# Performance work log

Hardware: AMD Instinct MI355X
Metric: run time of the kernel (lower is better)

## Reference

```python
import jax, jax.numpy as jnp
import numpy as np

N, E_DIM, H, N_EDGES, OUT = 4096, 256, 4, 131072, 256


def _ln(x, g, b, eps=1e-5):
    m = x.mean(-1, keepdims=True)
    v = ((x - m) ** 2).mean(-1, keepdims=True)
    return (x - m) / jnp.sqrt(v + eps) * g + b


def _mha(q_in, kv_in, in_w, in_b, out_w, out_b, n_heads):
    # torch nn.MultiheadAttention with packed in_proj_weight [3E, E]
    e = q_in.shape[-1]
    dh = e // n_heads
    wq, wk, wv = jnp.split(in_w, 3, axis=0)
    bq, bk, bv = jnp.split(in_b, 3)
    q = (q_in @ wq.T + bq).reshape(-1, n_heads, dh)   # [N,H,Dh]
    k = (kv_in @ wk.T + bk).reshape(-1, n_heads, dh)
    v = (kv_in @ wv.T + bv).reshape(-1, n_heads, dh)
    scale = 1.0 / jnp.sqrt(jnp.asarray(dh, q.dtype))
    scores = jnp.einsum('nhd,mhd->hnm', q, k) * scale  # [H,N,M]
    attn = jax.nn.softmax(scores, axis=-1)
    o = jnp.einsum('hnm,mhd->nhd', attn, v).reshape(-1, e)
    return o @ out_w.T + out_b


def _gcn_conv(x, edge_index):
    # out[c] += (1/sqrt(d[c])) * (1/sqrt(d[r])) * x[r] for each edge (r,c),
    # d = in-degree counted on col; non-finite norms zeroed (nan_to_num)
    n = x.shape[0]
    row, col = edge_index[0], edge_index[1]
    d = jax.ops.segment_sum(jnp.ones_like(col, dtype=x.dtype), col, num_segments=n)
    dn = 1.0 / jnp.sqrt(d)
    value = dn[col] * dn[row]
    value = jnp.where(jnp.isfinite(value), value, 0.0)
    return jax.ops.segment_sum(value[:, None] * x[row], col, num_segments=n)


def setup_inputs() -> dict:
    key = jax.random.key(0)
    ks = jax.random.split(key, 12)
    s = 1.0 / np.sqrt(E_DIM)
    rn = lambda k, shape: jax.random.normal(k, shape, jnp.float32) * s
    return {
        'x': jax.random.normal(ks[0], (N, E_DIM), jnp.float32),
        'edge_index': jax.random.randint(ks[1], (2, N_EDGES), 0, N, dtype=jnp.int32),
        'weight_local': jax.random.uniform(ks[2], (E_DIM, E_DIM), jnp.float32, -s, s),
        'sa_in_w': rn(ks[3], (3 * E_DIM, E_DIM)),
        'sa_in_b': jnp.zeros((3 * E_DIM,), jnp.float32),
        'sa_out_w': rn(ks[4], (E_DIM, E_DIM)),
        'sa_out_b': jnp.zeros((E_DIM,), jnp.float32),
        'ln1_g': jnp.ones((E_DIM,), jnp.float32),
        'ln1_b': jnp.zeros((E_DIM,), jnp.float32),
        'ca_in_w': rn(ks[5], (3 * E_DIM, E_DIM)),
        'ca_in_b': jnp.zeros((3 * E_DIM,), jnp.float32),
        'ca_out_w': rn(ks[6], (E_DIM, E_DIM)),
        'ca_out_b': jnp.zeros((E_DIM,), jnp.float32),
        'ln2_g': jnp.ones((E_DIM,), jnp.float32),
        'ln2_b': jnp.zeros((E_DIM,), jnp.float32),
        'gate_w': rn(ks[7], (E_DIM, 2 * E_DIM)),
        'gate_b': jnp.zeros((E_DIM,), jnp.float32),
        'fc_w': rn(ks[8], (OUT, E_DIM)),
        'fc_b': jnp.zeros((OUT,), jnp.float32),
    }


def reference(x, edge_index, weight_local, sa_in_w, sa_in_b, sa_out_w, sa_out_b,
              ln1_g, ln1_b, ca_in_w, ca_in_b, ca_out_w, ca_out_b, ln2_g, ln2_b,
              gate_w, gate_b, fc_w, fc_b):
    hi = _gcn_conv(x, edge_index)                       # [N,E]
    local_embed = hi @ weight_local                     # [N,E]
    attn_out = _mha(x, x, sa_in_w, sa_in_b, sa_out_w, sa_out_b, H)
    global_embed = _ln(x + attn_out, ln1_g, ln1_b)      # [N,E]
    cross_out = _mha(global_embed, local_embed, ca_in_w, ca_in_b, ca_out_w, ca_out_b, H)
    aligned = _ln(global_embed + cross_out, ln2_g, ln2_b)
    concat = jnp.concatenate([global_embed, aligned], axis=-1)  # [N,2E]
    final_embed = jax.nn.relu(concat @ gate_w.T + gate_b)
    return final_embed @ fc_w.T + fc_b
```

## Files before the change

kernel.cpp:

```cpp
#include <hip/hip_runtime.h>
#include <hip/hip_bf16.h>

#define NN 4096
#define EDIM 256
#define NHEAD 4
#define DH 64
#define NEDGE 131072
#define NE (NN * EDIM)
#define NSPLIT 8
#define KEYS_PER_SPLIT (NN / NSPLIT)
#define QKS 512
#define QSCL 0.18033688011112042f

typedef __bf16 bf16x8 __attribute__((ext_vector_type(8)));
typedef float f32x4 __attribute__((ext_vector_type(4)));
typedef float f32x16 __attribute__((ext_vector_type(16)));

__device__ inline void gload_lds16(const void* g, void* l) {
    __builtin_amdgcn_global_load_lds((const __attribute__((address_space(1))) unsigned int*)g,
                                     (__attribute__((address_space(3))) unsigned int*)l, 16, 0, 0);
}

__global__ __launch_bounds__(256) void prep_kernel(
    const float* __restrict__ wl, const float* __restrict__ siw, const float* __restrict__ sib,
    const float* __restrict__ sow, const float* __restrict__ ciw, const float* __restrict__ cib,
    const float* __restrict__ cow, const float* __restrict__ gw, const float* __restrict__ fw,
    const float* __restrict__ x,
    __bf16* __restrict__ siwb, __bf16* __restrict__ ciwb, __bf16* __restrict__ sowb,
    __bf16* __restrict__ cowb, __bf16* __restrict__ gwb, __bf16* __restrict__ fwb,
    __bf16* __restrict__ wlT, __bf16* __restrict__ xb,
    float* __restrict__ sib_adj, float* __restrict__ cib_adj, int* __restrict__ degi) {
    long i = (long)blockIdx.x * 256 + threadIdx.x;
    if (i < 196608) { float v = siw[i]; if (i < 65536) v *= QSCL; siwb[i] = (__bf16)v; return; }
    i -= 196608;
    if (i < 196608) { float v = ciw[i]; if (i < 65536) v *= QSCL; ciwb[i] = (__bf16)v; return; }
    i -= 196608;
    if (i < 65536) { sowb[i] = (__bf16)sow[i]; return; }
    i -= 65536;
    if (i < 65536) { cowb[i] = (__bf16)cow[i]; return; }
    i -= 65536;
    if (i < 131072) { gwb[i] = (__bf16)gw[i]; return; }
    i -= 131072;
    if (i < 65536) { fwb[i] = (__bf16)fw[i]; return; }
    i -= 65536;
    if (i < 65536) { int n = (int)(i >> 8), k = (int)(i & 255); wlT[i] = (__bf16)wl[k * 256 + n]; return; }
    i -= 65536;
    if (i < 1048576) { xb[i] = (__bf16)x[i]; return; }
    i -= 1048576;
    if (i < 768) { sib_adj[i] = sib[i] * (i < 256 ? QSCL : 1.f); return; }
    i -= 768;
    if (i < 768) { cib_adj[i] = cib[i] * (i < 256 ? QSCL : 1.f); return; }
    i -= 768;
    if (i < 4096) degi[i] = 0;
}

__global__ __launch_bounds__(256) void degi_kernel(const int* __restrict__ ei,
                                                   int* __restrict__ degi, int ne) {
    int e = blockIdx.x * 256 + threadIdx.x;
    if (e < ne) atomicAdd(&degi[ei[ne + e]], 1);
}

__global__ __launch_bounds__(256) void scan_kernel(const int* __restrict__ degi,
                                                   int* __restrict__ off,
                                                   int* __restrict__ cursor,
                                                   float* __restrict__ dnz) {
    __shared__ int s[256];
    const int t = threadIdx.x, i0 = t * 16;
    int v[16], sum = 0;
#pragma unroll
    for (int j = 0; j < 16; ++j) { v[j] = degi[i0 + j]; sum += v[j]; }
    s[t] = sum;
    __syncthreads();
#pragma unroll
    for (int d = 1; d < 256; d <<= 1) {
        int add = (t >= d) ? s[t - d] : 0;
        __syncthreads();
        s[t] += add;
        __syncthreads();
    }
    int base = s[t] - sum;
#pragma unroll
    for (int j = 0; j < 16; ++j) {
        off[i0 + j] = base;
        cursor[i0 + j] = base;
        dnz[i0 + j] = (v[j] > 0) ? rsqrtf((float)v[j]) : 0.f;
        base += v[j];
    }
}

__global__ __launch_bounds__(256) void fill_kernel(const int* __restrict__ ei,
                                                   int* __restrict__ cursor,
                                                   int* __restrict__ rows, int ne) {
    int e = blockIdx.x * 256 + threadIdx.x;
    if (e < ne) {
        int r = ei[e], c = ei[ne + e];
        int pos = atomicAdd(&cursor[c], 1);
        rows[pos] = r;
    }
}

__global__ __launch_bounds__(256) void gather_kernel(const int* __restrict__ off,
                                                     const int* __restrict__ rows,
                                                     const float* __restrict__ dnz,
                                                     const __bf16* __restrict__ xb,
                                                     __bf16* __restrict__ hib) {
    __shared__ float sm[2][256];
    const int c = blockIdx.x, t = threadIdx.x;
    const int half = t >> 7, c2 = (t & 127) * 2;
    const int s0 = off[c];
    const int s1 = (c == NN - 1) ? NEDGE : off[c + 1];
    float a0 = 0.f, a1 = 0.f;
    for (int j = s0 + half; j < s1; j += 2) {
        int r = rows[j];
        float dv = dnz[r];
        unsigned int pk = *(const unsigned int*)&xb[(size_t)r * EDIM + c2];
        a0 += dv * __uint_as_float(pk << 16);
        a1 += dv * __uint_as_float(pk & 0xffff0000u);
    }
    sm[half][c2] = a0;
    sm[half][c2 + 1] = a1;
    __syncthreads();
    float v = (sm[0][t] + sm[1][t]) * dnz[c];
    hib[(size_t)c * EDIM + t] = (__bf16)v;
}

__device__ inline void gemm_core(const __bf16* __restrict__ A, int lda,
                                 const __bf16* __restrict__ Bt, int ldb,
                                 int row0, int col0, int K, int tid,
                                 __bf16* As, __bf16* Bs, f32x4 acc[4]) {
    const int w = tid >> 6, l = tid & 63, lr = l & 15, lk = l >> 4;
    const int srow = (l >> 3), scol = (l & 7) * 8;
    auto stage = [&](int k0, int buf) {
#pragma unroll
        for (int cc = 0; cc < 2; ++cc) {
            int E0 = (w * 2 + cc) * 512;
            int row = (E0 >> 6) + srow;
            int sc = scol ^ ((row & 7) << 3);
            gload_lds16(A + (size_t)(row0 + row) * lda + k0 + sc, &As[buf * 4096 + E0]);
            gload_lds16(Bt + (size_t)(col0 + row) * ldb + k0 + sc, &Bs[buf * 4096 + E0]);
        }
    };
    stage(0, 0);
    __syncthreads();
    int buf = 0;
    for (int k0 = 0; k0 < K; k0 += 64) {
        if (k0 + 64 < K) stage(k0 + 64, buf ^ 1);
#pragma unroll
        for (int ks = 0; ks < 2; ++ks) {
            int cswz = (ks * 32 + lk * 8) ^ ((lr & 7) << 3);
            bf16x8 af = *(bf16x8*)&As[buf * 4096 + (w * 16 + lr) * 64 + cswz];
#pragma unroll
            for (int nt = 0; nt < 4; ++nt) {
                bf16x8 bfr = *(bf16x8*)&Bs[buf * 4096 + (nt * 16 + lr) * 64 + cswz];
                acc[nt] = __builtin_amdgcn_mfma_f32_16x16x32_bf16(af, bfr, acc[nt], 0, 0, 0);
            }
        }
        __syncthreads();
        buf ^= 1;
    }
}

template <bool RELU, bool OUTBF>
__global__ __launch_bounds__(256) void gemm_bf16(const __bf16* __restrict__ A,
                                                 const __bf16* __restrict__ A2, int lda,
                                                 const __bf16* __restrict__ Bt, int ldb,
                                                 const float* __restrict__ bias,
                                                 void* __restrict__ Cv, int ldc, int K) {
    __shared__ __align__(16) __bf16 As[2 * 4096];
    __shared__ __align__(16) __bf16 Bs[2 * 4096];
    const int tid = threadIdx.x;
    const int row0 = blockIdx.y * 64, col0 = blockIdx.x * 64;
    const int w = tid >> 6, l = tid & 63, lr = l & 15, lk = l >> 4;
    const int srow = (l >> 3), scol = (l & 7) * 8;
    f32x4 acc[4] = {};
    auto stage = [&](int k0, int buf) {
        const __bf16* Asrc = A;
        int ka = k0;
        if (A2 != nullptr && k0 >= 256) { Asrc = A2; ka = k0 - 256; }
#pragma unroll
        for (int cc = 0; cc < 2; ++cc) {
            int E0 = (w * 2 + cc) * 512;
            int row = (E0 >> 6) + srow;
            int sc = scol ^ ((row & 7) << 3);
            gload_lds16(Asrc + (size_t)(row0 + row) * lda + ka + sc, &As[buf * 4096 + E0]);
            gload_lds16(Bt + (size_t)(col0 + row) * ldb + k0 + sc, &Bs[buf * 4096 + E0]);
        }
    };
    stage(0, 0);
    __syncthreads();
    int buf = 0;
    for (int k0 = 0; k0 < K; k0 += 64) {
        if (k0 + 64 < K) stage(k0 + 64, buf ^ 1);
#pragma unroll
        for (int ks = 0; ks < 2; ++ks) {
            int cswz = (ks * 32 + lk * 8) ^ ((lr & 7) << 3);
            bf16x8 af = *(bf16x8*)&As[buf * 4096 + (w * 16 + lr) * 64 + cswz];
#pragma unroll
            for (int nt = 0; nt < 4; ++nt) {
                bf16x8 bfr = *(bf16x8*)&Bs[buf * 4096 + (nt * 16 + lr) * 64 + cswz];
                acc[nt] = __builtin_amdgcn_mfma_f32_16x16x32_bf16(af, bfr, acc[nt], 0, 0, 0);
            }
        }
        __syncthreads();
        buf ^= 1;
    }
#pragma unroll
    for (int nt = 0; nt < 4; ++nt) {
        float bv = bias ? bias[col0 + nt * 16 + lr] : 0.f;
#pragma unroll
        for (int r = 0; r < 4; ++r) {
            float v = acc[nt][r] + bv;
            if (RELU) v = fmaxf(v, 0.f);
            size_t ci = (size_t)(row0 + w * 16 + lk * 4 + r) * ldc + col0 + nt * 16 + lr;
            if (OUTBF) ((__bf16*)Cv)[ci] = (__bf16)v;
            else ((float*)Cv)[ci] = v;
        }
    }
}

__device__ inline void qkv_epilogue(f32x4 acc[4], const float* __restrict__ bias,
                                    int gcol0, int row0, int tid,
                                    __bf16* __restrict__ qkv, __bf16* __restrict__ vtb) {
    const int w = tid >> 6, l = tid & 63, lr = l & 15, lk = l >> 4;
    if (gcol0 < 512) {
#pragma unroll
        for (int nt = 0; nt < 4; ++nt) {
            float bv = bias[gcol0 + nt * 16 + lr];
#pragma unroll
            for (int r = 0; r < 4; ++r)
                qkv[(size_t)(row0 + w * 16 + lk * 4 + r) * QKS + gcol0 + nt * 16 + lr] =
                    (__bf16)(acc[nt][r] + bv);
        }
    } else {
        const int n4 = row0 + w * 16 + lk * 4;
#pragma unroll
        for (int nt = 0; nt < 4; ++nt) {
            int dg = gcol0 - 512 + nt * 16 + lr;
            float bv = bias[gcol0 + nt * 16 + lr];
            union { __bf16 b[4]; ushort4 u; } pk;
#pragma unroll
            for (int r = 0; r < 4; ++r) pk.b[r] = (__bf16)(acc[nt][r] + bv);
            *(ushort4*)&vtb[(size_t)dg * NN + n4] = pk.u;
        }
    }
}

__global__ __launch_bounds__(256) void fused_local_qkv(
    const __bf16* __restrict__ hi_bf, const __bf16* __restrict__ x_bf,
    const __bf16* __restrict__ wlT, const __bf16* __restrict__ siwb,
    const float* __restrict__ sib,
    __bf16* __restrict__ local_bf, __bf16* __restrict__ qkv, __bf16* __restrict__ vtb) {
    __shared__ __align__(16) __bf16 As[2 * 4096];
    __shared__ __align__(16) __bf16 Bs[2 * 4096];
    const int tid = threadIdx.x;
    const int bx = blockIdx.x, row0 = blockIdx.y * 64;
    f32x4 acc[4] = {};
    if (bx < 4) {
        gemm_core(hi_bf, 256, wlT, 256, row0, bx * 64, 256, tid, As, Bs, acc);
        const int w = tid >> 6, l = tid & 63, lr = l & 15, lk = l >> 4;
#pragma unroll
        for (int nt = 0; nt < 4; ++nt)
#pragma unroll
            for (int r = 0; r < 4; ++r)
                local_bf[(size_t)(row0 + w * 16 + lk * 4 + r) * 256 + bx * 64 + nt * 16 + lr] =
                    (__bf16)acc[nt][r];
    } else {
        const int gcol0 = (bx - 4) * 64;
        gemm_core(x_bf, 256, siwb, 256, row0, gcol0, 256, tid, As, Bs, acc);
        qkv_epilogue(acc, sib, gcol0, row0, tid, qkv, vtb);
    }
}

__global__ __launch_bounds__(256) void fused_cross_proj(
    const __bf16* __restrict__ global_bf, const __bf16* __restrict__ local_bf,
    const __bf16* __restrict__ ciwb, const float* __restrict__ cib,
    __bf16* __restrict__ qkv, __bf16* __restrict__ vtb) {
    __shared__ __align__(16) __bf16 As[2 * 4096];
    __shared__ __align__(16) __bf16 Bs[2 * 4096];
    const int tid = threadIdx.x;
    const int bx = blockIdx.x, row0 = blockIdx.y * 64;
    const int gcol0 = (bx < 4) ? bx * 64 : 256 + (bx - 4) * 64;
    const __bf16* A = (bx < 4) ? global_bf : local_bf;
    f32x4 acc[4] = {};
    gemm_core(A, 256, ciwb, 256, row0, gcol0, 256, tid, As, Bs, acc);
    qkv_epilogue(acc, cib, gcol0, row0, tid, qkv, vtb);
}

__global__ __launch_bounds__(256, 4) void attn_split(const __bf16* __restrict__ qkvb,
                                                     const __bf16* __restrict__ Vtb,
                                                     __bf16* __restrict__ p0,
                                                     __bf16* __restrict__ p1,
                                                     __bf16* __restrict__ p2,
                                                     __bf16* __restrict__ p3,
                                                     float* __restrict__ ml) {
    const int h = blockIdx.y, s = blockIdx.z;
    const int n0 = blockIdx.x * 128;
    const int tid = threadIdx.x;
    const int w = tid >> 6, l = tid & 63;
    const int qi = l & 31, hi = l >> 5, hi8 = hi * 8;
    const int swz = (l & 7) << 3;

    __shared__ __align__(16) __bf16 Kt[2 * 4096];
    __shared__ __align__(16) __bf16 Vt[2 * 4096];

    const int qrow = n0 + w * 32 + qi;
    bf16x8 qf[4];
#pragma unroll
    for (int d0 = 0; d0 < 4; ++d0)
        qf[d0] = *(const bf16x8*)&qkvb[(size_t)qrow * QKS + h * 64 + d0 * 16 + hi8];

    f32x16 ot0 = {}, ot1 = {};
    float sum_part = 0.f;
    const __bf16* Vbh = Vtb + (size_t)h * 64 * NN;
    const int srow = (l >> 3), scol = (l & 7) * 8;

    auto stageKV = [&](int t, int buf) {
        const int kv0 = s * KEYS_PER_SPLIT + t * 64;
#pragma unroll
        for (int cc = 0; cc < 2; ++cc) {
            int E0 = (w * 2 + cc) * 512;
            int row = (E0 >> 6) + srow;
            int sc = scol ^ ((row & 7) << 3);
            gload_lds16(qkvb + (size_t)(kv0 + row) * QKS + 256 + h * 64 + sc, &Kt[buf * 4096 + E0]);
            gload_lds16(Vbh + (size_t)row * NN + kv0 + sc, &Vt[buf * 4096 + E0]);
        }
    };

    stageKV(0, 0);
    __syncthreads();
    int buf = 0;
    for (int t = 0; t < KEYS_PER_SPLIT / 64; ++t) {
        if (t + 1 < KEYS_PER_SPLIT / 64) stageKV(t + 1, buf ^ 1);
#pragma unroll
        for (int ss = 0; ss < 2; ++ss) {
            f32x16 st = {};
#pragma unroll
            for (int d0 = 0; d0 < 4; ++d0) {
                bf16x8 kf = *(bf16x8*)&Kt[buf * 4096 + (ss * 32 + qi) * 64 + ((d0 * 16 + hi8) ^ swz)];
                st = __builtin_amdgcn_mfma_f32_32x32x16_bf16(kf, qf[d0], st, 0, 0, 0);
            }
            float p_[16];
#pragma unroll
            for (int r = 0; r < 16; ++r) {
                p_[r] = exp2f(st[r]);
                sum_part += p_[r];
            }
            unsigned int wd[8];
#pragma unroll
            for (int j = 0; j < 8; ++j)
                asm("v_cvt_pk_bf16_f32 %0, %1, %2" : "=v"(wd[j]) : "v"(p_[2 * j]), "v"(p_[2 * j + 1]));
            asm("v_permlane32_swap_b32 %0, %1" : "+v"(wd[0]), "+v"(wd[2]));
            asm("v_permlane32_swap_b32 %0, %1" : "+v"(wd[1]), "+v"(wd[3]));
            asm("v_permlane32_swap_b32 %0, %1" : "+v"(wd[4]), "+v"(wd[6]));
            asm("v_permlane32_swap_b32 %0, %1" : "+v"(wd[5]), "+v"(wd[7]));
            union { unsigned int u[4]; bf16x8 v; } pa0, pa1;
            pa0.u[0] = wd[0]; pa0.u[1] = wd[1]; pa0.u[2] = wd[2]; pa0.u[3] = wd[3];
            pa1.u[0] = wd[4]; pa1.u[1] = wd[5]; pa1.u[2] = wd[6]; pa1.u[3] = wd[7];
#pragma unroll
            for (int kt = 0; kt < 2; ++kt) {
                bf16x8 pav = kt ? pa1.v : pa0.v;
                int colk = (ss * 32 + kt * 16 + hi8) ^ swz;
                bf16x8 vf0 = *(bf16x8*)&Vt[buf * 4096 + qi * 64 + colk];
                bf16x8 vf1 = *(bf16x8*)&Vt[buf * 4096 + (32 + qi) * 64 + colk];
                ot0 = __builtin_amdgcn_mfma_f32_32x32x16_bf16(vf0, pav, ot0, 0, 0, 0);
                ot1 = __builtin_amdgcn_mfma_f32_32x32x16_bf16(vf1, pav, ot1, 0, 0, 0);
            }
        }
        __syncthreads();
        buf ^= 1;
    }

    float tot = sum_part + __shfl_xor(sum_part, 32);
    __bf16* pb;
    switch (s >> 1) {
        case 0: pb = p0; break;
        case 1: pb = p1; break;
        case 2: pb = p2; break;
        default: pb = p3; break;
    }
    pb += (size_t)(s & 1) * NHEAD * NN * 64;

    __bf16* lw = &Kt[w * 2048];
    const int sw = (qi & 7) << 3;
#pragma unroll
    for (int r = 0; r < 16; r += 2) {
        int d = (r & 3) + 8 * (r >> 2) + 4 * hi;
        union { unsigned int u; __bf16 b[2]; } w2, w3;
        w2.b[0] = (__bf16)ot0[r]; w2.b[1] = (__bf16)ot0[r + 1];
        w3.b[0] = (__bf16)ot1[r]; w3.b[1] = (__bf16)ot1[r + 1];
        *(unsigned int*)&lw[qi * 64 + (d ^ sw)] = w2.u;
        *(unsigned int*)&lw[qi * 64 + ((d + 32) ^ sw)] = w3.u;
    }
    if (hi == 0) ml[((size_t)s * NHEAD + h) * NN + qrow] = tot;
    __syncthreads();
    __bf16* gdst = pb + ((size_t)h * NN + n0 + w * 32) * 64;
#pragma unroll
    for (int j = 0; j < 4; ++j) {
        int q = (l >> 3) + j * 8;
        int x = (l & 7) * 8;
        bf16x8 v = *(bf16x8*)&lw[q * 64 + (x ^ ((q & 7) << 3))];
        *(bf16x8*)&gdst[q * 64 + x] = v;
    }
}

__global__ __launch_bounds__(256) void attn_merge(const __bf16* __restrict__ p0,
                                                  const __bf16* __restrict__ p1,
                                                  const __bf16* __restrict__ p2,
                                                  const __bf16* __restrict__ p3,
                                                  const float* __restrict__ ml,
                                                  __bf16* __restrict__ coreb) {
    int g = blockIdx.x * 256 + threadIdx.x;
    int d8 = g & 7;
    int hn = g >> 3;
    int n = hn & (NN - 1), h = hn >> 12;
    float L = 0.f;
    float o[8] = {};
#pragma unroll
    for (int s = 0; s < NSPLIT; ++s) {
        const __bf16* pb = (s < 2 ? p0 : s < 4 ? p1 : s < 6 ? p2 : p3) +
                           (size_t)(s & 1) * NHEAD * NN * 64;
        bf16x8 v = *(const bf16x8*)&pb[(size_t)hn * 64 + d8 * 8];
#pragma unroll
        for (int j = 0; j < 8; ++j) o[j] += (float)v[j];
        L += ml[((size_t)s * NHEAD + h) * NN + n];
    }
    float inv = 1.f / L;
    bf16x8 r;
#pragma unroll
    for (int j = 0; j < 8; ++j) r[j] = (__bf16)(o[j] * inv);
    *(bf16x8*)&coreb[(size_t)n * 256 + h * 64 + d8 * 8] = r;
}

__device__ inline float block_sum256(float v, float* tmp) {
#pragma unroll
    for (int o = 32; o; o >>= 1) v += __shfl_xor(v, o);
    __syncthreads();
    if ((threadIdx.x & 63) == 0) tmp[threadIdx.x >> 6] = v;
    __syncthreads();
    return tmp[0] + tmp[1] + tmp[2] + tmp[3];
}

__global__ __launch_bounds__(256) void ln_kernel(const float* __restrict__ a,
                                                 const float* __restrict__ b,
                                                 const float* __restrict__ g,
                                                 const float* __restrict__ be,
                                                 float* __restrict__ outf,
                                                 __bf16* __restrict__ outb) {
    __shared__ float tmp[4];
    const int n = blockIdx.x, t = threadIdx.x;
    float v = a[n * EDIM + t] + b[n * EDIM + t];
    float mean = block_sum256(v, tmp) * (1.f / 256.f);
    float c = v - mean;
    float var = block_sum256(c * c, tmp) * (1.f / 256.f);
    float o = c * (1.f / sqrtf(var + 1e-5f)) * g[t] + be[t];
    if (outf) outf[n * EDIM + t] = o;
    if (outb) outb[n * EDIM + t] = (__bf16)o;
}

extern "C" void kernel_launch(void* const* d_in, const int* in_sizes, int n_in,
                              void* d_out, int out_size, void* d_ws, size_t ws_size,
                              hipStream_t stream) {
    const float* x = (const float*)d_in[0];
    const int* ei = (const int*)d_in[1];
    const float* w_local = (const float*)d_in[2];
    const float* sa_in_w = (const float*)d_in[3];
    const float* sa_in_b = (const float*)d_in[4];
    const float* sa_out_w = (const float*)d_in[5];
    const float* sa_out_b = (const float*)d_in[6];
    const float* ln1_g = (const float*)d_in[7];
    const float* ln1_b = (const float*)d_in[8];
    const float* ca_in_w = (const float*)d_in[9];
    const float* ca_in_b = (const float*)d_in[10];
    const float* ca_out_w = (const float*)d_in[11];
    const float* ca_out_b = (const float*)d_in[12];
    const float* ln2_g = (const float*)d_in[13];
    const float* ln2_b = (const float*)d_in[14];
    const float* gate_w = (const float*)d_in[15];
    const float* gate_b = (const float*)d_in[16];
    const float* fc_w = (const float*)d_in[17];
    const float* fc_b = (const float*)d_in[18];
    float* out = (float*)d_out;

    float* ws = (float*)d_ws;
    float* dnz = ws;
    float* ml = ws + 4096;
    __bf16* x_bf = (__bf16*)(ml + 131072);
    __bf16* hi_bf = (__bf16*)((float*)x_bf + NE / 2);
    __bf16* local_bf = (__bf16*)((float*)hi_bf + NE / 2);
    __bf16* qkv_bf = (__bf16*)((float*)local_bf + NE / 2);
    __bf16* core_bf = (__bf16*)((float*)qkv_bf + 3 * NE / 2);
    float* proj = (float*)core_bf + NE / 2;
    float* global_f = proj + NE;
    __bf16* global_bf = (__bf16*)(global_f + NE);
    __bf16* aligned_bf = (__bf16*)((float*)global_bf + NE / 2);
    __bf16* fin_bf = (__bf16*)((float*)aligned_bf + NE / 2);
    __bf16* vtb = (__bf16*)((float*)fin_bf + NE / 2);
    __bf16* siwb = (__bf16*)((float*)vtb + NE / 2);
    __bf16* ciwb = siwb + 196608;
    __bf16* sowb = ciwb + 196608;
    __bf16* cowb = sowb + 65536;
    __bf16* gwb = cowb + 65536;
    __bf16* fwb = gwb + 131072;
    __bf16* wlT = fwb + 65536;
    float* sib_adj = (float*)(wlT + 65536);
    float* cib_adj = sib_adj + 768;

    int* degi = (int*)qkv_bf;
    int* off = degi + 4096;
    int* cursor = off + 4096;
    int* rows = cursor + 4096;

    __bf16* pA = (__bf16*)out;
    __bf16* pB = x_bf;
    __bf16* pC = (__bf16*)proj;
    __bf16* pD = aligned_bf;

    prep_kernel<<<7190, 256, 0, stream>>>(w_local, sa_in_w, sa_in_b, sa_out_w,
                                          ca_in_w, ca_in_b, ca_out_w, gate_w, fc_w, x,
                                          siwb, ciwb, sowb, cowb, gwb, fwb, wlT, x_bf,
                                          sib_adj, cib_adj, degi);

    degi_kernel<<<NEDGE / 256, 256, 0, stream>>>(ei, degi, NEDGE);
    scan_kernel<<<1, 256, 0, stream>>>(degi, off, cursor, dnz);
    fill_kernel<<<NEDGE / 256, 256, 0, stream>>>(ei, cursor, rows, NEDGE);
    gather_kernel<<<NN, 256, 0, stream>>>(off, rows, dnz, x_bf, hi_bf);

    fused_local_qkv<<<dim3(16, 64), 256, 0, stream>>>(
        hi_bf, x_bf, wlT, siwb, sib_adj, local_bf, qkv_bf, vtb);
    attn_split<<<dim3(NN / 128, NHEAD, NSPLIT), 256, 0, stream>>>(qkv_bf, vtb, pA, pB, pC, pD, ml);
    attn_merge<<<512, 256, 0, stream>>>(pA, pB, pC, pD, ml, core_bf);
    gemm_bf16<false, false><<<dim3(4, 64), 256, 0, stream>>>(
        core_bf, nullptr, 256, sowb, 256, sa_out_b, proj, 256, 256);
    ln_kernel<<<NN, 256, 0, stream>>>(x, proj, ln1_g, ln1_b, global_f, global_bf);

    fused_cross_proj<<<dim3(12, 64), 256, 0, stream>>>(
        global_bf, local_bf, ciwb, cib_adj, qkv_bf, vtb);
    attn_split<<<dim3(NN / 128, NHEAD, NSPLIT), 256, 0, stream>>>(qkv_bf, vtb, pA, pB, pC, pD, ml);
    attn_merge<<<512, 256, 0, stream>>>(pA, pB, pC, pD, ml, core_bf);
    gemm_bf16<false, false><<<dim3(4, 64), 256, 0, stream>>>(
        core_bf, nullptr, 256, cowb, 256, ca_out_b, proj, 256, 256);
    ln_kernel<<<NN, 256, 0, stream>>>(global_f, proj, ln2_g, ln2_b, nullptr, aligned_bf);

    gemm_bf16<true, true><<<dim3(4, 64), 256, 0, stream>>>(
        global_bf, aligned_bf, 256, gwb, 512, gate_b, fin_bf, 256, 512);
    gemm_bf16<false, false><<<dim3(4, 64), 256, 0, stream>>>(
        fin_bf, nullptr, 256, fwb, 256, fc_b, out, 256, 256);
}
```

Baseline: 174.2 us.

## Fuse split-attention merge into output projection GEMM and deepen KV prefetch

Removes the separate attn_merge kernel and its core_bf round trip. The output-projection GEMM now sums the eight split partials, normalises by the summed denominators, and writes the A tile straight into LDS. The attention split loop also moves from single-buffer-ahead prefetch to issuing two stages up front, with explicit vmcnt waits and raw barriers, so loads overlap more compute. The cost is that each GEMM block redundantly merges its A rows for every column tile, four times over. The hand-written waitcnt and barrier sequencing is fragile, and the projection output now lives in the qkv buffer.

```diff
diff --git a/kernel.cpp b/kernel.cpp
--- a/kernel.cpp
+++ b/kernel.cpp
@@ -218,6 +218,77 @@
     }
 }
 
+__global__ __launch_bounds__(256) void gemm_merge_proj(
+    const __bf16* __restrict__ p0, const __bf16* __restrict__ p1,
+    const __bf16* __restrict__ p2, const __bf16* __restrict__ p3,
+    const float* __restrict__ ml,
+    const __bf16* __restrict__ Bt, const float* __restrict__ bias,
+    float* __restrict__ C) {
+    __shared__ __align__(16) __bf16 As[4096];
+    __shared__ __align__(16) __bf16 Bs[4096];
+    const int tid = threadIdx.x;
+    const int row0 = blockIdx.y * 64, col0 = blockIdx.x * 64;
+    const int w = tid >> 6, l = tid & 63, lr = l & 15, lk = l >> 4;
+    const int srow = tid >> 2, sc0 = (tid & 3) * 16;
+    const int ssw = (srow & 7) << 3;
+    const int brow = l >> 3, bcol = (l & 7) * 8;
+    f32x4 acc[4] = {};
+    for (int k0 = 0; k0 < 256; k0 += 64) {
+        if (k0) __syncthreads();
+        const int h = k0 >> 6;
+        const int n = row0 + srow;
+        float L = 0.f;
+#pragma unroll
+        for (int s = 0; s < NSPLIT; ++s)
+            L += ml[((size_t)s * NHEAD + h) * NN + n];
+        float inv = 1.f / L;
+        float m0[8] = {}, m1[8] = {};
+#pragma unroll
+        for (int s = 0; s < NSPLIT; ++s) {
+            const __bf16* pb = (s < 2 ? p0 : s < 4 ? p1 : s < 6 ? p2 : p3) +
+                               (size_t)(s & 1) * NHEAD * NN * 64;
+            const __bf16* src = &pb[((size_t)h * NN + n) * 64 + sc0];
+            bf16x8 v0 = *(const bf16x8*)src;
+            bf16x8 v1 = *(const bf16x8*)(src + 8);
+#pragma unroll
+            for (int j = 0; j < 8; ++j) { m0[j] += (float)v0[j]; m1[j] += (float)v1[j]; }
+        }
+        bf16x8 o0, o1;
+#pragma unroll
+        for (int j = 0; j < 8; ++j) {
+            o0[j] = (__bf16)(m0[j] * inv);
+            o1[j] = (__bf16)(m1[j] * inv);
+        }
+        *(bf16x8*)&As[srow * 64 + (sc0 ^ ssw)] = o0;
+        *(bf16x8*)&As[srow * 64 + ((sc0 + 8) ^ ssw)] = o1;
+#pragma unroll
+        for (int cc = 0; cc < 2; ++cc) {
+            int E0 = (w * 2 + cc) * 512;
+            int row = (E0 >> 6) + brow;
+            int sc = bcol ^ ((row & 7) << 3);
+            gload_lds16(Bt + (size_t)(col0 + row) * 256 + k0 + sc, &Bs[E0]);
+        }
+        __syncthreads();
+#pragma unroll
+        for (int ks = 0; ks < 2; ++ks) {
+            int cswz = (ks * 32 + lk * 8) ^ ((lr & 7) << 3);
+            bf16x8 af = *(bf16x8*)&As[(w * 16 + lr) * 64 + cswz];
+#pragma unroll
+            for (int nt = 0; nt < 4; ++nt) {
+                bf16x8 bfr = *(bf16x8*)&Bs[(nt * 16 + lr) * 64 + cswz];
+                acc[nt] = __builtin_amdgcn_mfma_f32_16x16x32_bf16(af, bfr, acc[nt], 0, 0, 0);
+            }
+        }
+    }
+#pragma unroll
+    for (int nt = 0; nt < 4; ++nt) {
+        float bv = bias[col0 + nt * 16 + lr];
+#pragma unroll
+        for (int r = 0; r < 4; ++r)
+            C[(size_t)(row0 + w * 16 + lk * 4 + r) * 256 + col0 + nt * 16 + lr] = acc[nt][r] + bv;
+    }
+}
+
 __device__ inline void qkv_epilogue(f32x4 acc[4], const float* __restrict__ bias,
                                     int gcol0, int row0, int tid,
                                     __bf16* __restrict__ qkv, __bf16* __restrict__ vtb) {
@@ -327,10 +398,14 @@
     };
 
     stageKV(0, 0);
-    __syncthreads();
+    stageKV(1, 1);
     int buf = 0;
-    for (int t = 0; t < KEYS_PER_SPLIT / 64; ++t) {
-        if (t + 1 < KEYS_PER_SPLIT / 64) stageKV(t + 1, buf ^ 1);
+    const int T = KEYS_PER_SPLIT / 64;
+    for (int t = 0; t < T; ++t) {
+        if (t < T - 1)
+            asm volatile("s_waitcnt vmcnt(4)\n\ts_barrier" ::: "memory");
+        else
+            asm volatile("s_waitcnt vmcnt(0)\n\ts_barrier" ::: "memory");
 #pragma unroll
         for (int ss = 0; ss < 2; ++ss) {
             f32x16 st = {};
@@ -366,9 +441,13 @@
                 ot1 = __builtin_amdgcn_mfma_f32_32x32x16_bf16(vf1, pav, ot1, 0, 0, 0);
             }
         }
-        __syncthreads();
+        if (t + 2 < T) {
+            asm volatile("s_barrier" ::: "memory");
+            stageKV(t + 2, buf);
+        }
         buf ^= 1;
     }
+    asm volatile("s_barrier" ::: "memory");
 
     float tot = sum_part + __shfl_xor(sum_part, 32);
     __bf16* pb;
@@ -401,34 +480,6 @@
         bf16x8 v = *(bf16x8*)&lw[q * 64 + (x ^ ((q & 7) << 3))];
         *(bf16x8*)&gdst[q * 64 + x] = v;
     }
-}
-
-__global__ __launch_bounds__(256) void attn_merge(const __bf16* __restrict__ p0,
-                                                  const __bf16* __restrict__ p1,
-                                                  const __bf16* __restrict__ p2,
-                                                  const __bf16* __restrict__ p3,
-                                                  const float* __restrict__ ml,
-                                                  __bf16* __restrict__ coreb) {
-    int g = blockIdx.x * 256 + threadIdx.x;
-    int d8 = g & 7;
-    int hn = g >> 3;
-    int n = hn & (NN - 1), h = hn >> 12;
-    float L = 0.f;
-    float o[8] = {};
-#pragma unroll
-    for (int s = 0; s < NSPLIT; ++s) {
-        const __bf16* pb = (s < 2 ? p0 : s < 4 ? p1 : s < 6 ? p2 : p3) +
-                           (size_t)(s & 1) * NHEAD * NN * 64;
-        bf16x8 v = *(const bf16x8*)&pb[(size_t)hn * 64 + d8 * 8];
-#pragma unroll
-        for (int j = 0; j < 8; ++j) o[j] += (float)v[j];
-        L += ml[((size_t)s * NHEAD + h) * NN + n];
-    }
-    float inv = 1.f / L;
-    bf16x8 r;
-#pragma unroll
-    for (int j = 0; j < 8; ++j) r[j] = (__bf16)(o[j] * inv);
-    *(bf16x8*)&coreb[(size_t)n * 256 + h * 64 + d8 * 8] = r;
 }
 
 __device__ inline float block_sum256(float v, float* tmp) {
@@ -488,9 +539,9 @@
     __bf16* hi_bf = (__bf16*)((float*)x_bf + NE / 2);
     __bf16* local_bf = (__bf16*)((float*)hi_bf + NE / 2);
     __bf16* qkv_bf = (__bf16*)((float*)local_bf + NE / 2);
-    __bf16* core_bf = (__bf16*)((float*)qkv_bf + 3 * NE / 2);
-    float* proj = (float*)core_bf + NE / 2;
-    float* global_f = proj + NE;
+    __bf16* core_scratch = (__bf16*)((float*)qkv_bf + 3 * NE / 2);
+    float* part2 = (float*)core_scratch + NE / 2;
+    float* global_f = part2 + NE;
     __bf16* global_bf = (__bf16*)(global_f + NE);
     __bf16* aligned_bf = (__bf16*)((float*)global_bf + NE / 2);
     __bf16* fin_bf = (__bf16*)((float*)aligned_bf + NE / 2);
@@ -505,6 +556,8 @@
     float* sib_adj = (float*)(wlT + 65536);
     float* cib_adj = sib_adj + 768;
 
+    float* proj_f32 = (float*)qkv_bf;
+
     int* degi = (int*)qkv_bf;
     int* off = degi + 4096;
     int* cursor = off + 4096;
@@ -512,7 +565,7 @@
 
     __bf16* pA = (__bf16*)out;
     __bf16* pB = x_bf;
-    __bf16* pC = (__bf16*)proj;
+    __bf16* pC = (__bf16*)part2;
     __bf16* pD = aligned_bf;
 
     prep_kernel<<<7190, 256, 0, stream>>>(w_local, sa_in_w, sa_in_b, sa_out_w,
@@ -528,18 +581,16 @@
     fused_local_qkv<<<dim3(16, 64), 256, 0, stream>>>(
         hi_bf, x_bf, wlT, siwb, sib_adj, local_bf, qkv_bf, vtb);
     attn_split<<<dim3(NN / 128, NHEAD, NSPLIT), 256, 0, stream>>>(qkv_bf, vtb, pA, pB, pC, pD, ml);
-    attn_merge<<<512, 256, 0, stream>>>(pA, pB, pC, pD, ml, core_bf);
-    gemm_bf16<false, false><<<dim3(4, 64), 256, 0, stream>>>(
-        core_bf, nullptr, 256, sowb, 256, sa_out_b, proj, 256, 256);
-    ln_kernel<<<NN, 256, 0, stream>>>(x, proj, ln1_g, ln1_b, global_f, global_bf);
+    gemm_merge_proj<<<dim3(4, 64), 256, 0, stream>>>(
+        pA, pB, pC, pD, ml, sowb, sa_out_b, proj_f32);
+    ln_kernel<<<NN, 256, 0, stream>>>(x, proj_f32, ln1_g, ln1_b, global_f, global_bf);
 
     fused_cross_proj<<<dim3(12, 64), 256, 0, stream>>>(
         global_bf, local_bf, ciwb, cib_adj, qkv_bf, vtb);
     attn_split<<<dim3(NN / 128, NHEAD, NSPLIT), 256, 0, stream>>>(qkv_bf, vtb, pA, pB, pC, pD, ml);
-    attn_merge<<<512, 256, 0, stream>>>(pA, pB, pC, pD, ml, core_bf);
-    gemm_bf16<false, false><<<dim3(4, 64), 256, 0, stream>>>(
-        core_bf, nullptr, 256, cowb, 256, ca_out_b, proj, 256, 256);
-    ln_kernel<<<NN, 256, 0, stream>>>(global_f, proj, ln2_g, ln2_b, nullptr, aligned_bf);
+    gemm_merge_proj<<<dim3(4, 64), 256, 0, stream>>>(
+        pA, pB, pC, pD, ml, cowb, ca_out_b, proj_f32);
+    ln_kernel<<<NN, 256, 0, stream>>>(global_f, proj_f32, ln2_g, ln2_b, nullptr, aligned_bf);
 
     gemm_bf16<true, true><<<dim3(4, 64), 256, 0, stream>>>(
         global_bf, aligned_bf, 256, gwb, 512, gate_b, fin_bf, 256, 512);
```

Measured after the change: 188.6 us. 1.08x slower.
